# Kernel optimization log

Measured on AMD Instinct MI355X. Metric: run time of the kernel, lower is better.

Reference implementation:

```python
import jax, jax.numpy as jnp
import numpy as np

N = 12288
D = 64
K = 16
EPS = 1e-5
DIAG_BIAS = 1e6


def setup_inputs() -> dict:
    key = jax.random.key(0)
    k1, k2 = jax.random.split(key)
    coords = jax.random.normal(k1, (N, D), dtype=jnp.float32)
    potential = jax.random.normal(k2, (N,), dtype=jnp.float32)
    return {"coords": coords, "potential": potential, "k": K}


def reference(coords, potential, k):
    # Pairwise squared distances: ||xi - xj||^2 + eps  (same math as (diff**2).sum(-1))
    sq = jnp.sum(coords * coords, axis=1)                      # (N,)
    dist2 = sq[:, None] + sq[None, :] - 2.0 * (coords @ coords.T) + EPS  # (N, N)
    n = coords.shape[0]
    dist2 = dist2 + jnp.eye(n, dtype=coords.dtype) * DIAG_BIAS  # exclude self
    # kNN via top-k of negated distances (matches torch.topk(-dist2, k, dim=1))
    knn_vals, knn_idx = jax.lax.top_k(-dist2, k)                # (N, k) each
    sigma2 = jnp.mean(dist2)                                    # scalar (incl. diag bias, as in source)
    weights = jnp.exp(knn_vals / (sigma2 + EPS))                # (N, k)
    v_nb = potential[knn_idx]                                   # (N, k) gather
    lap = jnp.sum(weights * (v_nb - potential[:, None]), axis=1)  # (N,)
    return lap
```

## Files before the change

kernel.cpp:

```cpp
#include <hip/hip_runtime.h>
#include <hip/hip_bf16.h>

#define N_PTS 12288
#define DIM   64
#define KSEL  16
#define EPS_F 1e-5f
#define TMARGIN 2.0f

typedef __bf16 bf16x8 __attribute__((ext_vector_type(8)));
typedef float  f32x4  __attribute__((ext_vector_type(4)));

__device__ __forceinline__ void grid_sync(int* bar)
{
    __syncthreads();
    if (threadIdx.x == 0) {
        __hip_atomic_fetch_add(bar, 1, __ATOMIC_RELEASE, __HIP_MEMORY_SCOPE_AGENT);
        while (__hip_atomic_load(bar, __ATOMIC_ACQUIRE, __HIP_MEMORY_SCOPE_AGENT)
               < (int)gridDim.x)
            __builtin_amdgcn_s_sleep(2);
    }
    __syncthreads();
}

template<int CVN>
__device__ __forceinline__ void rank_core(const unsigned* __restrict__ drow,
                                          int S, int l32, int* __restrict__ fj)
{
    unsigned cv[CVN]; int rk[CVN];
    #pragma unroll
    for (int t = 0; t < CVN; ++t) {
        cv[t] = (t * 32 + l32 < S) ? drow[t * 32 + l32] : 0xFFFFFFFFu;
        rk[t] = 0;
    }
    #pragma unroll 4
    for (int m = 0; m < S; ++m) {
        const unsigned o = drow[m];
        #pragma unroll
        for (int t = 0; t < CVN; ++t) rk[t] += (o < cv[t]) ? 1 : 0;
    }
    #pragma unroll
    for (int t = 0; t < CVN; ++t)
        if (rk[t] < 32 && cv[t] != 0xFFFFFFFFu)
            fj[rk[t]] = (int)(cv[t] & 0x3FFFu);
}

__global__ __launch_bounds__(512) void mega_kernel(
    const float* __restrict__ coords,
    const float* __restrict__ pot,
    float* __restrict__ s1,
    float* __restrict__ sx,
    int* __restrict__ bar,
    __hip_bfloat16* __restrict__ chi,
    __hip_bfloat16* __restrict__ chiX,
    float* __restrict__ out)
{
    constexpr int ROWS = 48, TIL = 3, CAPP = 8, OCAP = 16;
    constexpr int SEGS = 32;
    constexpr int DCAP = SEGS * CAPP + OCAP;
    constexpr int DPAD = DCAP + 1;
    constexpr int JSL  = N_PTS / 8;
    constexpr int STEPS = JSL / 16;

    __shared__ float    colsh[8][64];
    __shared__ float    sqs8[8];
    __shared__ float    sqloc[ROWS];
    __shared__ float    pool[ROWS][64];
    __shared__ float    TrowS[ROWS];
    __shared__ unsigned buf[TIL * CAPP * 512];
    __shared__ int      cntT[TIL][8][4][16];
    __shared__ unsigned dense[ROWS * DPAD];
    __shared__ unsigned ovf[ROWS][OCAP];
    __shared__ int      ovcnt[ROWS];
    __shared__ int      stotS[ROWS];
    __shared__ int      finj[16][32];
    __shared__ double   refd[16][32];
    __shared__ double   s_inv_den;

    const int tid  = threadIdx.x;
    const int lane = tid & 63;
    const int wave = tid >> 6;
    const int col  = lane & 15;
    const int quad = lane >> 4;
    const int ibase = (int)blockIdx.x * ROWS;

    float colsum = 0.f, sqsum = 0.f;
    #pragma unroll 1
    for (int k = 0; k < 6; ++k) {
        const int rl = wave * 6 + k, gr = ibase + rl;
        const float x = coords[gr * DIM + lane];
        chi[gr * DIM + lane] = __float2bfloat16(x);
        colsum += x;
        float p = x * x;
        #pragma unroll
        for (int off = 32; off > 0; off >>= 1) p += __shfl_xor(p, off, 64);
        if (lane == 0) { sqloc[rl] = p; sqsum += p; }
        if (lane < 8) {
            const __hip_bfloat16 h = __float2bfloat16(p);
            const float lo = p - (float)h;
            __hip_bfloat16 v;
            if (lane == 0)      v = h;
            else if (lane == 1) v = __float2bfloat16(lo);
            else if (lane < 4)  v = __float2bfloat16(1.0f);
            else                v = __float2bfloat16(0.0f);
            chiX[gr * 8 + lane] = v;
        }
    }
    colsh[wave][lane] = colsum;
    if (lane == 0) sqs8[wave] = sqsum;
    if (tid < ROWS) ovcnt[tid] = 0;
    __syncthreads();
    if (wave == 0) {
        float c = 0.f;
        #pragma unroll
        for (int w8 = 0; w8 < 8; ++w8) c += colsh[w8][lane];
        atomicAdd(&sx[lane], c);
    }
    if (tid == 0) {
        float t = 0.f;
        #pragma unroll
        for (int w8 = 0; w8 < 8; ++w8) t += sqs8[w8];
        atomicAdd(s1, t);
    }
    grid_sync(bar);

    if (tid == 0) {
        double S1 = (double)s1[0], m2 = 0.0;
        for (int d = 0; d < DIM; ++d) { double t = (double)sx[d]; m2 += t * t; }
        const double NN = (double)N_PTS;
        s_inv_den = 1.0 / ((2.0 * NN * S1 - 2.0 * m2) / (NN * NN)
                           + 1e-5 + 1e6 / NN + 1e-5);
    }

    const bf16x8* cp  = (const bf16x8*)chi;
    const bf16x8* cpX = (const bf16x8*)chiX;
    bf16x8 bA[TIL], bB[TIL], b2[TIL];
    #pragma unroll
    for (int t = 0; t < TIL; ++t) {
        const int it = ibase + t * 16 + col;
        bA[t] = cp[it * 8 + quad];
        bB[t] = cp[it * 8 + quad + 4];
        bf16x8 v;
        #pragma unroll
        for (int e = 0; e < 8; ++e) v[e] = (__bf16)0.0f;
        if (quad == 0) {
            const float bs = sqloc[t * 16 + col] + EPS_F;
            const __bf16 bh = (__bf16)(0.5f * bs);
            const __bf16 bl = (__bf16)(0.5f * bs - (float)bh);
            v[0] = (__bf16)(-0.5f); v[1] = (__bf16)(-0.5f);
            v[2] = (__bf16)(-(float)bh); v[3] = (__bf16)(-(float)bl);
        }
        b2[t] = v;
    }

    const int jw  = wave * JSL;
    const int seg = wave * 4 + quad;

    auto LD = [&](int s, bf16x8& A0, bf16x8& A1, bf16x8& A2) {
        const int ar = jw + s * 16 + col;
        A0 = cp[ar * 8 + quad];
        A1 = cp[ar * 8 + quad + 4];
        A2 = cpX[ar];
    };
    auto MFMA3 = [&](const bf16x8& A0, const bf16x8& A1, const bf16x8& A2,
                     f32x4 (&acc)[TIL]) {
        #pragma unroll
        for (int t = 0; t < TIL; ++t) {
            f32x4 a = {0.f, 0.f, 0.f, 0.f};
            a = __builtin_amdgcn_mfma_f32_16x16x32_bf16(A0, bA[t], a, 0, 0, 0);
            a = __builtin_amdgcn_mfma_f32_16x16x32_bf16(A1, bB[t], a, 0, 0, 0);
            a = __builtin_amdgcn_mfma_f32_16x16x32_bf16(A2, b2[t], a, 0, 0, 0);
            acc[t] = a;
        }
    };

    float m0[TIL], m1[TIL];
    #pragma unroll
    for (int t = 0; t < TIL; ++t) { m0[t] = -1e30f; m1[t] = -1e30f; }
    {
        bf16x8 A0[4], A1[4], A2[4];
        #pragma unroll
        for (int p = 0; p < 4; ++p) LD(2 * p, A0[p], A1[p], A2[p]);
        #pragma unroll 1
        for (int k = 0; k < STEPS / 2; k += 4) {
            #pragma unroll
            for (int p = 0; p < 4; ++p) {
                f32x4 acc[TIL];
                MFMA3(A0[p], A1[p], A2[p], acc);
                int sn = 2 * (k + p + 4);
                sn = (sn < STEPS) ? sn : 0;
                LD(sn, A0[p], A1[p], A2[p]);
                #pragma unroll
                for (int t = 0; t < TIL; ++t) {
                    #pragma unroll
                    for (int r = 0; r < 4; ++r) {
                        const float da = acc[t][r];
                        const bool g = da > m0[t];
                        m1[t] = g ? m0[t] : fmaxf(m1[t], da);
                        m0[t] = fmaxf(m0[t], da);
                    }
                }
            }
        }
    }
    #pragma unroll
    for (int t = 0; t < TIL; ++t) {
        pool[t * 16 + col][seg * 2]     = -2.f * m0[t];
        pool[t * 16 + col][seg * 2 + 1] = -2.f * m1[t];
    }
    __syncthreads();

    #pragma unroll 1
    for (int rr = 0; rr < 6; ++rr) {
        const int row = wave * 6 + rr;
        const float val = pool[row][lane];
        int rank = 0;
        #pragma unroll 8
        for (int m = 0; m < 64; ++m) {
            const float o = pool[row][m];
            rank += (o < val || (o == val && m < lane)) ? 1 : 0;
        }
        if (rank == 16) TrowS[row] = val + TMARGIN;
    }
    __syncthreads();

    float tthr[TIL];
    #pragma unroll
    for (int t = 0; t < TIL; ++t) tthr[t] = -0.5f * TrowS[t * 16 + col];

    int ct[TIL] = {0, 0, 0};
    {
        bf16x8 A0[4], A1[4], A2[4];
        #pragma unroll
        for (int p = 0; p < 4; ++p) LD(p, A0[p], A1[p], A2[p]);
        #pragma unroll 1
        for (int s = 0; s < STEPS; s += 4) {
            #pragma unroll
            for (int p = 0; p < 4; ++p) {
                f32x4 acc[TIL];
                MFMA3(A0[p], A1[p], A2[p], acc);
                int sn = s + p + 4;
                sn = (sn < STEPS) ? sn : 0;
                LD(sn, A0[p], A1[p], A2[p]);

                const int jq = jw + (s + p) * 16 + quad * 4;
                #pragma unroll
                for (int t = 0; t < TIL; ++t) {
                    const float mx = fmaxf(fmaxf(acc[t][0], acc[t][1]),
                                           fmaxf(acc[t][2], acc[t][3]));
                    if (mx > tthr[t]) {
                        if (__all(ct[t] <= CAPP - 4)) {
                            #pragma unroll
                            for (int r = 0; r < 4; ++r) {
                                const float d2 = -2.f * acc[t][r];
                                const unsigned pk =
                                    (__float_as_uint(d2) & 0xFFFFC000u)
                                    | (unsigned)(jq + r);
                                buf[(t * CAPP + ct[t]) * 512 + tid] = pk;
                                ct[t] += (acc[t][r] > tthr[t]) ? 1 : 0;
                            }
                        } else {
                            #pragma unroll
                            for (int r = 0; r < 4; ++r) {
                                if (acc[t][r] > tthr[t]) {
                                    const float d2 = -2.f * acc[t][r];
                                    const unsigned pk =
                                        (__float_as_uint(d2) & 0xFFFFC000u)
                                        | (unsigned)(jq + r);
                                    if (ct[t] < CAPP) {
                                        buf[(t * CAPP + ct[t]) * 512 + tid] = pk;
                                        ++ct[t];
                                    } else {
                                        const int row = t * 16 + col;
                                        const int sl = atomicAdd(&ovcnt[row], 1);
                                        if (sl < OCAP) ovf[row][sl] = pk;
                                    }
                                }
                            }
                        }
                    }
                }
            }
        }
    }
    cntT[0][wave][quad][col] = ct[0];
    cntT[1][wave][quad][col] = ct[1];
    cntT[2][wave][quad][col] = ct[2];
    __syncthreads();

    {
        int bs[TIL] = {0, 0, 0}, tot[TIL] = {0, 0, 0};
        #pragma unroll 4
        for (int sg = 0; sg < SEGS; ++sg) {
            #pragma unroll
            for (int t = 0; t < TIL; ++t) {
                const int c = cntT[t][sg >> 2][sg & 3][col];
                if (sg < seg) bs[t] += c;
                tot[t] += c;
            }
        }
        #pragma unroll
        for (int t = 0; t < TIL; ++t)
            for (int p = 0; p < ct[t]; ++p)
                dense[(t * 16 + col) * DPAD + bs[t] + p] = buf[(t * CAPP + p) * 512 + tid];
        if (wave == 0 && quad == 0) {
            #pragma unroll
            for (int t = 0; t < TIL; ++t) {
                const int row = t * 16 + col;
                const int ov = ovcnt[row] < OCAP ? ovcnt[row] : OCAP;
                for (int o = 0; o < ov; ++o) dense[row * DPAD + tot[t] + o] = ovf[row][o];
                stotS[row] = tot[t] + ov;
            }
        }
    }
    __syncthreads();

    const double inv_den = s_inv_den;
    const int hw  = tid >> 5;
    const int l32 = tid & 31;
    #pragma unroll 1
    for (int pass = 0; pass < 3; ++pass) {
        const int row  = pass * 16 + hw;
        const int grow = ibase + row;
        const int S    = stotS[row];
        finj[hw][l32] = grow;

        const unsigned* drow = dense + row * DPAD;
        if (S <= 96) rank_core<3>(drow, S, l32, finj[hw]);
        else         rank_core<9>(drow, S, l32, finj[hw]);
        __syncthreads();

        const int j = finj[hw][l32];
        const float4* xi = (const float4*)(coords + grow * DIM);
        const float4* xj = (const float4*)(coords + j * DIM);
        double dot = 0.0, sqi = 0.0, sqj = 0.0;
        #pragma unroll
        for (int q = 0; q < DIM / 4; ++q) {
            const float4 a = xi[q], b = xj[q];
            dot += (double)a.x * (double)b.x + (double)a.y * (double)b.y
                 + (double)a.z * (double)b.z + (double)a.w * (double)b.w;
            sqi += (double)a.x * (double)a.x + (double)a.y * (double)a.y
                 + (double)a.z * (double)a.z + (double)a.w * (double)a.w;
            sqj += (double)b.x * (double)b.x + (double)b.y * (double)b.y
                 + (double)b.z * (double)b.z + (double)b.w * (double)b.w;
        }
        double d2 = sqi + sqj + 1e-5 - 2.0 * dot;
        if (j == grow) d2 = 1e300;
        refd[hw][l32] = d2;
        __syncthreads();

        int rank = 0;
        #pragma unroll 1
        for (int m = 0; m < 32; ++m) {
            const double o = refd[hw][m];
            rank += (o < d2 || (o == d2 && m < l32)) ? 1 : 0;
        }
        const double wgt = exp(-d2 * inv_den);
        double contrib = (rank < KSEL && j != grow)
                       ? wgt * ((double)pot[j] - (double)pot[grow]) : 0.0;
        #pragma unroll
        for (int off = 1; off < 32; off <<= 1)
            contrib += __shfl_xor(contrib, off, 64);
        if (l32 == 0) out[grow] = (float)contrib;
        __syncthreads();
    }
}

extern "C" void kernel_launch(void* const* d_in, const int* in_sizes, int n_in,
                              void* d_out, int out_size, void* d_ws, size_t ws_size,
                              hipStream_t stream)
{
    (void)in_sizes; (void)n_in; (void)out_size; (void)ws_size;
    const float* coords = (const float*)d_in[0];
    const float* pot    = (const float*)d_in[1];

    char* w = (char*)d_ws;
    float* s1 = (float*)w;
    float* sx = (float*)(w + 4);
    int*   bar = (int*)(w + 512);
    __hip_bfloat16* chi  = (__hip_bfloat16*)(w + 1024);
    __hip_bfloat16* chiX = (__hip_bfloat16*)(w + 1024 + (size_t)N_PTS * DIM * 2);

    hipMemsetAsync((void*)w, 0, 1024, stream);
    mega_kernel<<<dim3(N_PTS / 48), dim3(512), 0, stream>>>(
        coords, pot, s1, sx, bar, chi, chiX, (float*)d_out);
}
```

Before: 200.6 us.

## Switch distance GEMM to 32x32x16 MFMA with atomic candidate collection

Replaces the 16x16x32 bf16 MFMA tiling (three 16-row tiles) with 32x32x16 MFMAs over two 32-row tiles, the second tile half-padded, and widens the norm-augmentation vector to 16 entries. The threshold pre-pass now samples a quarter of each wave's column slice and keeps top-2 per 32-lane half, giving 32 pool entries per row instead of 64. Candidate collection drops the per-thread register buffers, prefix-sum compaction and overflow lists in favour of direct LDS atomicAdd into a per-row dense array. This aims for higher MFMA throughput and less bookkeeping, at the cost of wasted MFMA work on the padded tile, a sparser threshold sample that may admit more candidates, and LDS atomic contention.

New measurement: 237.1 us. 18.1% more time.

```diff
diff --git a/kernel.cpp b/kernel.cpp
--- a/kernel.cpp
+++ b/kernel.cpp
@@ -8,7 +8,7 @@
 #define TMARGIN 2.0f
 
 typedef __bf16 bf16x8 __attribute__((ext_vector_type(8)));
-typedef float  f32x4  __attribute__((ext_vector_type(4)));
+typedef float  f32x16 __attribute__((ext_vector_type(16)));
 
 __device__ __forceinline__ void grid_sync(int* bar)
 {
@@ -54,24 +54,17 @@
     __hip_bfloat16* __restrict__ chiX,
     float* __restrict__ out)
 {
-    constexpr int ROWS = 48, TIL = 3, CAPP = 8, OCAP = 16;
-    constexpr int SEGS = 32;
-    constexpr int DCAP = SEGS * CAPP + OCAP;
-    constexpr int DPAD = DCAP + 1;
+    constexpr int ROWS = 48, DCAP = 256, DPAD = 257;
     constexpr int JSL  = N_PTS / 8;
-    constexpr int STEPS = JSL / 16;
+    constexpr int STEPS = JSL / 32;
 
     __shared__ float    colsh[8][64];
     __shared__ float    sqs8[8];
     __shared__ float    sqloc[ROWS];
-    __shared__ float    pool[ROWS][64];
+    __shared__ float    pool[ROWS][32];
     __shared__ float    TrowS[ROWS];
-    __shared__ unsigned buf[TIL * CAPP * 512];
-    __shared__ int      cntT[TIL][8][4][16];
     __shared__ unsigned dense[ROWS * DPAD];
-    __shared__ unsigned ovf[ROWS][OCAP];
-    __shared__ int      ovcnt[ROWS];
-    __shared__ int      stotS[ROWS];
+    __shared__ int      cnt[ROWS];
     __shared__ int      finj[16][32];
     __shared__ double   refd[16][32];
     __shared__ double   s_inv_den;
@@ -79,8 +72,8 @@
     const int tid  = threadIdx.x;
     const int lane = tid & 63;
     const int wave = tid >> 6;
-    const int col  = lane & 15;
-    const int quad = lane >> 4;
+    const int l31  = lane & 31;
+    const int half = lane >> 5;
     const int ibase = (int)blockIdx.x * ROWS;
 
     float colsum = 0.f, sqsum = 0.f;
@@ -94,20 +87,20 @@
         #pragma unroll
         for (int off = 32; off > 0; off >>= 1) p += __shfl_xor(p, off, 64);
         if (lane == 0) { sqloc[rl] = p; sqsum += p; }
-        if (lane < 8) {
-            const __hip_bfloat16 h = __float2bfloat16(p);
-            const float lo = p - (float)h;
-            __hip_bfloat16 v;
-            if (lane == 0)      v = h;
-            else if (lane == 1) v = __float2bfloat16(lo);
+        if (lane < 16) {
+            __hip_bfloat16 v = __float2bfloat16(0.0f);
+            if (lane == 0)      v = __float2bfloat16(p);
+            else if (lane == 1) {
+                const float h = (float)__float2bfloat16(p);
+                v = __float2bfloat16(p - h);
+            }
             else if (lane < 4)  v = __float2bfloat16(1.0f);
-            else                v = __float2bfloat16(0.0f);
-            chiX[gr * 8 + lane] = v;
+            chiX[gr * 16 + lane] = v;
         }
     }
     colsh[wave][lane] = colsum;
     if (lane == 0) sqs8[wave] = sqsum;
-    if (tid < ROWS) ovcnt[tid] = 0;
+    if (tid < ROWS) cnt[tid] = 0;
     __syncthreads();
     if (wave == 0) {
         float c = 0.f;
@@ -133,200 +126,160 @@
 
     const bf16x8* cp  = (const bf16x8*)chi;
     const bf16x8* cpX = (const bf16x8*)chiX;
-    bf16x8 bA[TIL], bB[TIL], b2[TIL];
+    bf16x8 zf;
     #pragma unroll
-    for (int t = 0; t < TIL; ++t) {
-        const int it = ibase + t * 16 + col;
-        bA[t] = cp[it * 8 + quad];
-        bB[t] = cp[it * 8 + quad + 4];
-        bf16x8 v;
-        #pragma unroll
-        for (int e = 0; e < 8; ++e) v[e] = (__bf16)0.0f;
-        if (quad == 0) {
-            const float bs = sqloc[t * 16 + col] + EPS_F;
+    for (int e = 0; e < 8; ++e) zf[e] = (__bf16)0.0f;
+
+    bf16x8 Bf[2][5];
+    const int  i0r = ibase + l31;
+    const bool t1v = (l31 < 16);
+    const int  i1r = ibase + 32 + (l31 & 15);
+    #pragma unroll
+    for (int m = 0; m < 4; ++m) {
+        Bf[0][m] = cp[i0r * 8 + 2 * m + half];
+        Bf[1][m] = t1v ? cp[i1r * 8 + 2 * m + half] : zf;
+    }
+    {
+        bf16x8 v = zf;
+        if (half == 0) {
+            const float bs = sqloc[l31] + EPS_F;
             const __bf16 bh = (__bf16)(0.5f * bs);
             const __bf16 bl = (__bf16)(0.5f * bs - (float)bh);
             v[0] = (__bf16)(-0.5f); v[1] = (__bf16)(-0.5f);
             v[2] = (__bf16)(-(float)bh); v[3] = (__bf16)(-(float)bl);
         }
-        b2[t] = v;
-    }
-
-    const int jw  = wave * JSL;
-    const int seg = wave * 4 + quad;
-
-    auto LD = [&](int s, bf16x8& A0, bf16x8& A1, bf16x8& A2) {
-        const int ar = jw + s * 16 + col;
-        A0 = cp[ar * 8 + quad];
-        A1 = cp[ar * 8 + quad + 4];
-        A2 = cpX[ar];
+        Bf[0][4] = v;
+        v = zf;
+        if (half == 0 && t1v) {
+            const float bs = sqloc[32 + l31] + EPS_F;
+            const __bf16 bh = (__bf16)(0.5f * bs);
+            const __bf16 bl = (__bf16)(0.5f * bs - (float)bh);
+            v[0] = (__bf16)(-0.5f); v[1] = (__bf16)(-0.5f);
+            v[2] = (__bf16)(-(float)bh); v[3] = (__bf16)(-(float)bl);
+        }
+        Bf[1][4] = v;
+    }
+
+    const int jw = wave * JSL;
+    const f32x16 Z = {0.f,0.f,0.f,0.f,0.f,0.f,0.f,0.f,
+                      0.f,0.f,0.f,0.f,0.f,0.f,0.f,0.f};
+
+    auto LDA = [&](int s, bf16x8 (&A)[5]) {
+        const int jr = jw + s * 32 + l31;
+        A[0] = cp[jr * 8 + half];
+        A[1] = cp[jr * 8 + 2 + half];
+        A[2] = cp[jr * 8 + 4 + half];
+        A[3] = cp[jr * 8 + 6 + half];
+        A[4] = cpX[jr * 2 + half];
     };
-    auto MFMA3 = [&](const bf16x8& A0, const bf16x8& A1, const bf16x8& A2,
-                     f32x4 (&acc)[TIL]) {
-        #pragma unroll
-        for (int t = 0; t < TIL; ++t) {
-            f32x4 a = {0.f, 0.f, 0.f, 0.f};
-            a = __builtin_amdgcn_mfma_f32_16x16x32_bf16(A0, bA[t], a, 0, 0, 0);
-            a = __builtin_amdgcn_mfma_f32_16x16x32_bf16(A1, bB[t], a, 0, 0, 0);
-            a = __builtin_amdgcn_mfma_f32_16x16x32_bf16(A2, b2[t], a, 0, 0, 0);
-            acc[t] = a;
+    auto ACC2 = [&](const bf16x8 (&A)[5], f32x16& a0, f32x16& a1) {
+        a0 = __builtin_amdgcn_mfma_f32_32x32x16_bf16(A[0], Bf[0][0], Z, 0, 0, 0);
+        a1 = __builtin_amdgcn_mfma_f32_32x32x16_bf16(A[0], Bf[1][0], Z, 0, 0, 0);
+        #pragma unroll
+        for (int m = 1; m < 5; ++m) {
+            a0 = __builtin_amdgcn_mfma_f32_32x32x16_bf16(A[m], Bf[0][m], a0, 0, 0, 0);
+            a1 = __builtin_amdgcn_mfma_f32_32x32x16_bf16(A[m], Bf[1][m], a1, 0, 0, 0);
         }
     };
 
-    float m0[TIL], m1[TIL];
-    #pragma unroll
-    for (int t = 0; t < TIL; ++t) { m0[t] = -1e30f; m1[t] = -1e30f; }
+    float p00 = -1e30f, p01 = -1e30f, p10 = -1e30f, p11 = -1e30f;
+    auto TOP2 = [&](const f32x16& a, float& m0, float& m1) {
+        #pragma unroll
+        for (int r = 0; r < 16; ++r) {
+            const float v = a[r];
+            const bool g = v > m0;
+            m1 = g ? m0 : fmaxf(m1, v);
+            m0 = fmaxf(m0, v);
+        }
+    };
     {
-        bf16x8 A0[4], A1[4], A2[4];
-        #pragma unroll
-        for (int p = 0; p < 4; ++p) LD(2 * p, A0[p], A1[p], A2[p]);
+        bf16x8 Aa[5], Ab[5];
+        LDA(0, Aa); LDA(4, Ab);
         #pragma unroll 1
-        for (int k = 0; k < STEPS / 2; k += 4) {
-            #pragma unroll
-            for (int p = 0; p < 4; ++p) {
-                f32x4 acc[TIL];
-                MFMA3(A0[p], A1[p], A2[p], acc);
-                int sn = 2 * (k + p + 4);
-                sn = (sn < STEPS) ? sn : 0;
-                LD(sn, A0[p], A1[p], A2[p]);
-                #pragma unroll
-                for (int t = 0; t < TIL; ++t) {
-                    #pragma unroll
-                    for (int r = 0; r < 4; ++r) {
-                        const float da = acc[t][r];
-                        const bool g = da > m0[t];
-                        m1[t] = g ? m0[t] : fmaxf(m1[t], da);
-                        m0[t] = fmaxf(m0[t], da);
-                    }
-                }
-            }
-        }
-    }
-    #pragma unroll
-    for (int t = 0; t < TIL; ++t) {
-        pool[t * 16 + col][seg * 2]     = -2.f * m0[t];
-        pool[t * 16 + col][seg * 2 + 1] = -2.f * m1[t];
-    }
-    __syncthreads();
-
-    #pragma unroll 1
-    for (int rr = 0; rr < 6; ++rr) {
-        const int row = wave * 6 + rr;
-        const float val = pool[row][lane];
-        int rank = 0;
-        #pragma unroll 8
-        for (int m = 0; m < 64; ++m) {
-            const float o = pool[row][m];
-            rank += (o < val || (o == val && m < lane)) ? 1 : 0;
-        }
-        if (rank == 16) TrowS[row] = val + TMARGIN;
-    }
-    __syncthreads();
-
-    float tthr[TIL];
-    #pragma unroll
-    for (int t = 0; t < TIL; ++t) tthr[t] = -0.5f * TrowS[t * 16 + col];
-
-    int ct[TIL] = {0, 0, 0};
+        for (int k = 0; k < 12; k += 2) {
+            { f32x16 a0, a1; ACC2(Aa, a0, a1);
+              int sn = (k + 2) * 4; LDA(sn < STEPS ? sn : 0, Aa);
+              TOP2(a0, p00, p01); TOP2(a1, p10, p11); }
+            { f32x16 a0, a1; ACC2(Ab, a0, a1);
+              int sn = (k + 3) * 4; LDA(sn < STEPS ? sn : 0, Ab);
+              TOP2(a0, p00, p01); TOP2(a1, p10, p11); }
+        }
+    }
     {
-        bf16x8 A0[4], A1[4], A2[4];
-        #pragma unroll
-        for (int p = 0; p < 4; ++p) LD(p, A0[p], A1[p], A2[p]);
-        #pragma unroll 1
-        for (int s = 0; s < STEPS; s += 4) {
-            #pragma unroll
-            for (int p = 0; p < 4; ++p) {
-                f32x4 acc[TIL];
-                MFMA3(A0[p], A1[p], A2[p], acc);
-                int sn = s + p + 4;
-                sn = (sn < STEPS) ? sn : 0;
-                LD(sn, A0[p], A1[p], A2[p]);
-
-                const int jq = jw + (s + p) * 16 + quad * 4;
-                #pragma unroll
-                for (int t = 0; t < TIL; ++t) {
-                    const float mx = fmaxf(fmaxf(acc[t][0], acc[t][1]),
-                                           fmaxf(acc[t][2], acc[t][3]));
-                    if (mx > tthr[t]) {
-                        if (__all(ct[t] <= CAPP - 4)) {
-                            #pragma unroll
-                            for (int r = 0; r < 4; ++r) {
-                                const float d2 = -2.f * acc[t][r];
-                                const unsigned pk =
-                                    (__float_as_uint(d2) & 0xFFFFC000u)
-                                    | (unsigned)(jq + r);
-                                buf[(t * CAPP + ct[t]) * 512 + tid] = pk;
-                                ct[t] += (acc[t][r] > tthr[t]) ? 1 : 0;
-                            }
-                        } else {
-                            #pragma unroll
-                            for (int r = 0; r < 4; ++r) {
-                                if (acc[t][r] > tthr[t]) {
-                                    const float d2 = -2.f * acc[t][r];
-                                    const unsigned pk =
-                                        (__float_as_uint(d2) & 0xFFFFC000u)
-                                        | (unsigned)(jq + r);
-                                    if (ct[t] < CAPP) {
-                                        buf[(t * CAPP + ct[t]) * 512 + tid] = pk;
-                                        ++ct[t];
-                                    } else {
-                                        const int row = t * 16 + col;
-                                        const int sl = atomicAdd(&ovcnt[row], 1);
-                                        if (sl < OCAP) ovf[row][sl] = pk;
-                                    }
-                                }
-                            }
-                        }
-                    }
-                }
-            }
-        }
-    }
-    cntT[0][wave][quad][col] = ct[0];
-    cntT[1][wave][quad][col] = ct[1];
-    cntT[2][wave][quad][col] = ct[2];
-    __syncthreads();
-
-    {
-        int bs[TIL] = {0, 0, 0}, tot[TIL] = {0, 0, 0};
-        #pragma unroll 4
-        for (int sg = 0; sg < SEGS; ++sg) {
-            #pragma unroll
-            for (int t = 0; t < TIL; ++t) {
-                const int c = cntT[t][sg >> 2][sg & 3][col];
-                if (sg < seg) bs[t] += c;
-                tot[t] += c;
-            }
-        }
-        #pragma unroll
-        for (int t = 0; t < TIL; ++t)
-            for (int p = 0; p < ct[t]; ++p)
-                dense[(t * 16 + col) * DPAD + bs[t] + p] = buf[(t * CAPP + p) * 512 + tid];
-        if (wave == 0 && quad == 0) {
-            #pragma unroll
-            for (int t = 0; t < TIL; ++t) {
-                const int row = t * 16 + col;
-                const int ov = ovcnt[row] < OCAP ? ovcnt[row] : OCAP;
-                for (int o = 0; o < ov; ++o) dense[row * DPAD + tot[t] + o] = ovf[row][o];
-                stotS[row] = tot[t] + ov;
-            }
-        }
-    }
-    __syncthreads();
-
-    const double inv_den = s_inv_den;
+        const int slot = wave * 4 + half * 2;
+        pool[l31][slot]     = -2.f * p00;
+        pool[l31][slot + 1] = -2.f * p01;
+        if (t1v) {
+            pool[32 + l31][slot]     = -2.f * p10;
+            pool[32 + l31][slot + 1] = -2.f * p11;
+        }
+    }
+    __syncthreads();
+
     const int hw  = tid >> 5;
     const int l32 = tid & 31;
     #pragma unroll 1
     for (int pass = 0; pass < 3; ++pass) {
+        const int row = pass * 16 + hw;
+        const float val = pool[row][l32];
+        int rank = 0;
+        #pragma unroll 8
+        for (int m = 0; m < 32; ++m) {
+            const float o = pool[row][m];
+            rank += (o < val || (o == val && m < l32)) ? 1 : 0;
+        }
+        if (rank == 16) TrowS[row] = val + TMARGIN;
+    }
+    __syncthreads();
+
+    const float tthr0 = -0.5f * TrowS[l31];
+    const float tthr1 = t1v ? -0.5f * TrowS[32 + l31] : 1e30f;
+
+    auto EPI = [&](int s, const f32x16& a, float tthr, int lrow) {
+        float mx = fmaxf(fmaxf(fmaxf(a[0], a[1]), fmaxf(a[2], a[3])),
+                         fmaxf(fmaxf(a[4], a[5]), fmaxf(a[6], a[7])));
+        mx = fmaxf(mx, fmaxf(fmaxf(fmaxf(a[8], a[9]),  fmaxf(a[10], a[11])),
+                             fmaxf(fmaxf(a[12], a[13]), fmaxf(a[14], a[15]))));
+        if (mx > tthr) {
+            const int jb = jw + s * 32 + 4 * half;
+            #pragma unroll
+            for (int r = 0; r < 16; ++r) {
+                if (a[r] > tthr) {
+                    const float d2 = -2.f * a[r];
+                    const unsigned pk = (__float_as_uint(d2) & 0xFFFFC000u)
+                                      | (unsigned)(jb + (r & 3) + 8 * (r >> 2));
+                    const int idx = atomicAdd(&cnt[lrow], 1);
+                    if (idx < DCAP) dense[lrow * DPAD + idx] = pk;
+                }
+            }
+        }
+    };
+    {
+        bf16x8 Aa[5], Ab[5];
+        LDA(0, Aa); LDA(1, Ab);
+        #pragma unroll 1
+        for (int s = 0; s < STEPS; s += 2) {
+            { f32x16 a0, a1; ACC2(Aa, a0, a1);
+              int sn = s + 2; LDA(sn < STEPS ? sn : 0, Aa);
+              EPI(s, a0, tthr0, l31); EPI(s, a1, tthr1, 32 + (l31 & 15)); }
+            { f32x16 a0, a1; ACC2(Ab, a0, a1);
+              int sn = s + 3; LDA(sn < STEPS ? sn : 0, Ab);
+              EPI(s + 1, a0, tthr0, l31); EPI(s + 1, a1, tthr1, 32 + (l31 & 15)); }
+        }
+    }
+    __syncthreads();
+
+    const double inv_den = s_inv_den;
+    #pragma unroll 1
+    for (int pass = 0; pass < 3; ++pass) {
         const int row  = pass * 16 + hw;
         const int grow = ibase + row;
-        const int S    = stotS[row];
+        int S = cnt[row]; S = S < DCAP ? S : DCAP;
         finj[hw][l32] = grow;
 
         const unsigned* drow = dense + row * DPAD;
         if (S <= 96) rank_core<3>(drow, S, l32, finj[hw]);
-        else         rank_core<9>(drow, S, l32, finj[hw]);
+        else         rank_core<8>(drow, S, l32, finj[hw]);
         __syncthreads();
 
         const int j = finj[hw][l32];
```

## Software-pipeline MFMA and candidate epilogue, sparsify threshold sampling, alias pool into dense

Applied to the files above, without the earlier changes.

The candidate-filtering pass now alternates two accumulator sets, so the threshold/packing epilogue for one step runs while the MFMAs for the next step are issued. The threshold-estimation pass samples every fourth step instead of every second, which halves that pre-pass. The pool scratch array is aliased onto the dense LDS buffer to save shared memory, and per-thread and overflow capacities grow, with the larger rank_core variant to match. The packed key now stores the raw accumulator instead of -2*acc. That changes the sort-key encoding, and the sparser sample may give a looser threshold and more candidates.

Measured after the change: 225.3 us. 12.3% more time.

```diff
diff --git a/kernel.cpp b/kernel.cpp
--- a/kernel.cpp
+++ b/kernel.cpp
@@ -54,7 +54,7 @@
     __hip_bfloat16* __restrict__ chiX,
     float* __restrict__ out)
 {
-    constexpr int ROWS = 48, TIL = 3, CAPP = 8, OCAP = 16;
+    constexpr int ROWS = 48, TIL = 3, CAPP = 10, OCAP = 32;
     constexpr int SEGS = 32;
     constexpr int DCAP = SEGS * CAPP + OCAP;
     constexpr int DPAD = DCAP + 1;
@@ -64,17 +64,18 @@
     __shared__ float    colsh[8][64];
     __shared__ float    sqs8[8];
     __shared__ float    sqloc[ROWS];
-    __shared__ float    pool[ROWS][64];
     __shared__ float    TrowS[ROWS];
     __shared__ unsigned buf[TIL * CAPP * 512];
     __shared__ int      cntT[TIL][8][4][16];
-    __shared__ unsigned dense[ROWS * DPAD];
+    __shared__ __align__(16) unsigned dense[ROWS * DPAD];
     __shared__ unsigned ovf[ROWS][OCAP];
     __shared__ int      ovcnt[ROWS];
     __shared__ int      stotS[ROWS];
     __shared__ int      finj[16][32];
     __shared__ double   refd[16][32];
     __shared__ double   s_inv_den;
+
+    float (*pool)[64] = (float (*)[64])dense;
 
     const int tid  = threadIdx.x;
     const int lane = tid & 63;
@@ -179,14 +180,14 @@
     {
         bf16x8 A0[4], A1[4], A2[4];
         #pragma unroll
-        for (int p = 0; p < 4; ++p) LD(2 * p, A0[p], A1[p], A2[p]);
+        for (int p = 0; p < 4; ++p) LD(4 * p, A0[p], A1[p], A2[p]);
         #pragma unroll 1
-        for (int k = 0; k < STEPS / 2; k += 4) {
+        for (int k = 0; k < 24; k += 4) {
             #pragma unroll
             for (int p = 0; p < 4; ++p) {
                 f32x4 acc[TIL];
                 MFMA3(A0[p], A1[p], A2[p], acc);
-                int sn = 2 * (k + p + 4);
+                int sn = 4 * (k + p + 4);
                 sn = (sn < STEPS) ? sn : 0;
                 LD(sn, A0[p], A1[p], A2[p]);
                 #pragma unroll
@@ -228,59 +229,69 @@
     for (int t = 0; t < TIL; ++t) tthr[t] = -0.5f * TrowS[t * 16 + col];
 
     int ct[TIL] = {0, 0, 0};
-    {
-        bf16x8 A0[4], A1[4], A2[4];
-        #pragma unroll
-        for (int p = 0; p < 4; ++p) LD(p, A0[p], A1[p], A2[p]);
-        #pragma unroll 1
-        for (int s = 0; s < STEPS; s += 4) {
-            #pragma unroll
-            for (int p = 0; p < 4; ++p) {
-                f32x4 acc[TIL];
-                MFMA3(A0[p], A1[p], A2[p], acc);
-                int sn = s + p + 4;
-                sn = (sn < STEPS) ? sn : 0;
-                LD(sn, A0[p], A1[p], A2[p]);
-
-                const int jq = jw + (s + p) * 16 + quad * 4;
-                #pragma unroll
-                for (int t = 0; t < TIL; ++t) {
-                    const float mx = fmaxf(fmaxf(acc[t][0], acc[t][1]),
-                                           fmaxf(acc[t][2], acc[t][3]));
-                    if (mx > tthr[t]) {
-                        if (__all(ct[t] <= CAPP - 4)) {
-                            #pragma unroll
-                            for (int r = 0; r < 4; ++r) {
-                                const float d2 = -2.f * acc[t][r];
-                                const unsigned pk =
-                                    (__float_as_uint(d2) & 0xFFFFC000u)
-                                    | (unsigned)(jq + r);
+    auto EPI = [&](int s, const f32x4 (&acc)[TIL]) {
+        const int jq = jw + s * 16 + quad * 4;
+        #pragma unroll
+        for (int t = 0; t < TIL; ++t) {
+            const float mx = fmaxf(fmaxf(acc[t][0], acc[t][1]),
+                                   fmaxf(acc[t][2], acc[t][3]));
+            if (mx > tthr[t]) {
+                if (__all(ct[t] <= CAPP - 4)) {
+                    #pragma unroll
+                    for (int r = 0; r < 4; ++r) {
+                        const unsigned pk =
+                            (__float_as_uint(acc[t][r]) & 0xFFFFC000u)
+                            | (unsigned)(jq + r);
+                        buf[(t * CAPP + ct[t]) * 512 + tid] = pk;
+                        ct[t] += (acc[t][r] > tthr[t]) ? 1 : 0;
+                    }
+                } else {
+                    #pragma unroll
+                    for (int r = 0; r < 4; ++r) {
+                        if (acc[t][r] > tthr[t]) {
+                            const unsigned pk =
+                                (__float_as_uint(acc[t][r]) & 0xFFFFC000u)
+                                | (unsigned)(jq + r);
+                            if (ct[t] < CAPP) {
                                 buf[(t * CAPP + ct[t]) * 512 + tid] = pk;
-                                ct[t] += (acc[t][r] > tthr[t]) ? 1 : 0;
-                            }
-                        } else {
-                            #pragma unroll
-                            for (int r = 0; r < 4; ++r) {
-                                if (acc[t][r] > tthr[t]) {
-                                    const float d2 = -2.f * acc[t][r];
-                                    const unsigned pk =
-                                        (__float_as_uint(d2) & 0xFFFFC000u)
-                                        | (unsigned)(jq + r);
-                                    if (ct[t] < CAPP) {
-                                        buf[(t * CAPP + ct[t]) * 512 + tid] = pk;
-                                        ++ct[t];
-                                    } else {
-                                        const int row = t * 16 + col;
-                                        const int sl = atomicAdd(&ovcnt[row], 1);
-                                        if (sl < OCAP) ovf[row][sl] = pk;
-                                    }
-                                }
+                                ++ct[t];
+                            } else {
+                                const int row = t * 16 + col;
+                                const int sl = atomicAdd(&ovcnt[row], 1);
+                                if (sl < OCAP) ovf[row][sl] = pk;
                             }
                         }
                     }
                 }
             }
         }
+    };
+    {
+        bf16x8 A0[4], A1[4], A2[4];
+        #pragma unroll
+        for (int p = 0; p < 4; ++p) LD(p, A0[p], A1[p], A2[p]);
+        f32x4 X[TIL], Y[TIL];
+        MFMA3(A0[0], A1[0], A2[0], X);
+        LD(4, A0[0], A1[0], A2[0]);
+        #pragma unroll 1
+        for (int s = 0; s < STEPS - 4; s += 4) {
+            MFMA3(A0[1], A1[1], A2[1], Y);
+            { int sn = s + 5; sn = sn < STEPS ? sn : 0; LD(sn, A0[1], A1[1], A2[1]); }
+            EPI(s, X);
+            MFMA3(A0[2], A1[2], A2[2], X);
+            { int sn = s + 6; sn = sn < STEPS ? sn : 0; LD(sn, A0[2], A1[2], A2[2]); }
+            EPI(s + 1, Y);
+            MFMA3(A0[3], A1[3], A2[3], Y);
+            { int sn = s + 7; sn = sn < STEPS ? sn : 0; LD(sn, A0[3], A1[3], A2[3]); }
+            EPI(s + 2, X);
+            MFMA3(A0[0], A1[0], A2[0], X);
+            { int sn = s + 8; sn = sn < STEPS ? sn : 0; LD(sn, A0[0], A1[0], A2[0]); }
+            EPI(s + 3, Y);
+        }
+        MFMA3(A0[1], A1[1], A2[1], Y); EPI(STEPS - 4, X);
+        MFMA3(A0[2], A1[2], A2[2], X); EPI(STEPS - 3, Y);
+        MFMA3(A0[3], A1[3], A2[3], Y); EPI(STEPS - 2, X);
+        EPI(STEPS - 1, Y);
     }
     cntT[0][wave][quad][col] = ct[0];
     cntT[1][wave][quad][col] = ct[1];
@@ -326,7 +337,7 @@
 
         const unsigned* drow = dense + row * DPAD;
         if (S <= 96) rank_core<3>(drow, S, l32, finj[hw]);
-        else         rank_core<9>(drow, S, l32, finj[hw]);
+        else         rank_core<11>(drow, S, l32, finj[hw]);
         __syncthreads();
 
         const int j = finj[hw][l32];
```
